# Performance work log

Measured on AMD Instinct MI355X. Metric: run time of the kernel, lower is better.

## Reference

```python
import jax, jax.numpy as jnp
import numpy as np

N = 50000   # nodes
E = 600000  # edges (avg degree 12)
F = 16      # raw node features
P = 32      # n_channels_preproc
C = 128     # n_channels
L = 6       # n_gnn_layers
LBL = 2     # n_labels


def _dense_init(k, fan_in, shape):
    return (jax.random.normal(k, shape, jnp.float32) / np.float32(np.sqrt(fan_in)))


def setup_inputs() -> dict:
    key = jax.random.key(0)
    ks = jax.random.split(key, 12)
    return {
        "x": jax.random.normal(ks[0], (N, F), jnp.float32),
        "edge_src": jax.random.randint(ks[1], (E,), 0, N, dtype=jnp.int32),
        "edge_dst": jax.random.randint(ks[2], (E,), 0, N, dtype=jnp.int32),
        "edge_weight": jax.random.uniform(ks[3], (E,), jnp.float32),  # normalized-adjacency values
        "preproc_W": _dense_init(ks[4], F, (F, P)), "preproc_b": jnp.zeros((P,), jnp.float32),
        "fc_in1_W": _dense_init(ks[5], P, (P, C)), "fc_in1_b": jnp.zeros((C,), jnp.float32),
        "fc_in2_W": _dense_init(ks[6], P, (P, C)), "fc_in2_b": jnp.zeros((C,), jnp.float32),
        "gcn_W": _dense_init(ks[7], C, (L, C, C)), "gcn_b": jnp.zeros((L, C), jnp.float32),
        "fcg_W": _dense_init(ks[8], 2 * C, (L, 2 * C, C)), "fcg_b": jnp.zeros((L, C), jnp.float32),
        "last1_W": _dense_init(ks[9], 2 * C, (2 * C, C)), "last1_b": jnp.zeros((C,), jnp.float32),
        "last2_W": _dense_init(ks[10], C, (C, LBL)), "last2_b": jnp.zeros((LBL,), jnp.float32),
    }


def reference(x, edge_src, edge_dst, edge_weight,
              preproc_W, preproc_b, fc_in1_W, fc_in1_b, fc_in2_W, fc_in2_b,
              gcn_W, gcn_b, fcg_W, fcg_b, last1_W, last1_b, last2_W, last2_b):
    relu = jax.nn.relu
    h = relu(x @ preproc_W + preproc_b)                      # preproc Dense
    node_id = relu(h @ fc_in1_W + fc_in1_b)                  # node identity branch
    h = relu(h @ fc_in2_W + fc_in2_b)

    def layer(h, params):
        W, b, Wf, bf = params
        # GCNConv: act(A_hat @ (h @ W) + b), A_hat as COO edge list
        hw = h @ W                                           # [N, C]
        msg = hw[edge_src] * edge_weight[:, None]            # [E, C]
        agg = jax.ops.segment_sum(msg, edge_dst, num_segments=N)
        g = relu(agg + b)
        merged = jnp.concatenate([node_id, g], axis=-1)      # [N, 2C]
        return relu(merged @ Wf + bf), None                  # dropout = identity (eval)

    h, _ = jax.lax.scan(layer, h, (gcn_W, gcn_b, fcg_W, fcg_b))

    merged = jnp.concatenate([node_id, h], axis=-1)
    h = relu(merged @ last1_W + last1_b)
    return jax.nn.sigmoid(h @ last2_W + last2_b)             # [N, n_labels]
```

## Files before the change

kernel.cpp:

```cpp
#include <hip/hip_runtime.h>
#include <cstddef>
#include <cstdint>

#define NN 50000
#define NE 600000
#define NB 391

typedef __attribute__((ext_vector_type(8))) short bf16x8;
typedef __attribute__((ext_vector_type(4))) float f32x4;

#define SWZ(x) (((x) ^ ((x) >> 2)) & 3)

#define GLDS16(src, dst)                                                     \
    __builtin_amdgcn_global_load_lds(                                        \
        (const __attribute__((address_space(1))) void*)(src),                \
        (__attribute__((address_space(3))) void*)(dst), 16, 0, 0)

__device__ __forceinline__ float bf2f(ushort u) {
    return __uint_as_float(((uint32_t)u) << 16);
}
__device__ __forceinline__ ushort f2bf(float f) {
    uint32_t b = __float_as_uint(f);
    return (ushort)((b + 0x7FFF + ((b >> 16) & 1)) >> 16);
}

__global__ __launch_bounds__(256)
void convbh_kernel(const float* __restrict__ f1W, const float* __restrict__ f2W,
                   const float* __restrict__ gW, const float* __restrict__ fgW,
                   const float* __restrict__ l1W, ushort* __restrict__ wt,
                   const int* __restrict__ dst, int* __restrict__ bcnt)
{
    if (blockIdx.x < 1312) {
        int i = blockIdx.x * 256 + threadIdx.x;
        if (i >= 335872) return;
        float v;
        if (i < 4096) {
            int c = i >> 5, k = i & 31;
            v = f1W[k * 128 + c];
        } else if (i < 8192) {
            int j = i - 4096; int c = j >> 5, k = j & 31;
            v = f2W[k * 128 + c];
        } else if (i < 8192 + 98304) {
            int j = i - 8192; int l = j >> 14, r = j & 16383;
            int c = r >> 7, k = r & 127;
            v = gW[l * 16384 + k * 128 + c];
        } else if (i < 8192 + 98304 + 196608) {
            int j = i - (8192 + 98304); int l = j >> 15, r = j & 32767;
            int c = r >> 8, k = r & 255;
            v = fgW[l * 32768 + k * 128 + c];
        } else {
            int j = i - (8192 + 98304 + 196608);
            int c = j >> 8, k = j & 255;
            v = l1W[k * 128 + c];
        }
        wt[i] = f2bf(v);
    } else {
        __shared__ int h[NB];
        int tx = threadIdx.x;
        for (int i = tx; i < NB; i += 256) h[i] = 0;
        __syncthreads();
        int e0 = (blockIdx.x - 1312) * 1024;
#pragma unroll
        for (int k = 0; k < 4; ++k) {
            int e = e0 + k * 256 + tx;
            if (e < NE) atomicAdd(&h[dst[e] >> 7], 1);
        }
        __syncthreads();
        for (int i = tx; i < NB; i += 256)
            if (h[i]) atomicAdd(&bcnt[i], h[i]);
    }
}

__global__ __launch_bounds__(512)
void bscan_kernel(const int* __restrict__ bcnt, int* __restrict__ bbase,
                  int* __restrict__ bcur)
{
    __shared__ int buf[512];
    int t = threadIdx.x;
    int v = (t < NB) ? bcnt[t] : 0;
    buf[t] = v;
    __syncthreads();
    for (int s = 1; s < 512; s <<= 1) {
        int u = (t >= s) ? buf[t - s] : 0;
        __syncthreads();
        buf[t] += u;
        __syncthreads();
    }
    if (t < NB) {
        int ex = buf[t] - v;
        bbase[t] = ex;
        bcur[t]  = ex;
    }
    if (t == 0) bbase[NB] = NE;
}

__global__ __launch_bounds__(256)
void pass1_kernel(const int* __restrict__ src, const int* __restrict__ dst,
                  const float* __restrict__ w, int* __restrict__ bcur,
                  unsigned int* __restrict__ stage_pk,
                  unsigned char* __restrict__ stage_dl)
{
    __shared__ int cnt[NB];
    __shared__ int gbase[NB];
    int tx = threadIdx.x;
    for (int i = tx; i < NB; i += 256) cnt[i] = 0;
    __syncthreads();
    int e0 = blockIdx.x * 1024;
    int myd[4], myrank[4];
    unsigned int mypk[4];
#pragma unroll
    for (int k = 0; k < 4; ++k) {
        int e = e0 + k * 256 + tx;
        if (e < NE) {
            int d = dst[e];
            myd[k]    = d;
            mypk[k]   = (unsigned int)src[e] | ((unsigned int)f2bf(w[e]) << 17);
            myrank[k] = atomicAdd(&cnt[d >> 7], 1);
        } else {
            myd[k] = -1;
        }
    }
    __syncthreads();
    for (int i = tx; i < NB; i += 256)
        gbase[i] = cnt[i] ? atomicAdd(&bcur[i], cnt[i]) : 0;
    __syncthreads();
#pragma unroll
    for (int k = 0; k < 4; ++k) {
        if (myd[k] >= 0) {
            int p = gbase[myd[k] >> 7] + myrank[k];
            stage_pk[p] = mypk[k];
            stage_dl[p] = (unsigned char)(myd[k] & 127);
        }
    }
}

__global__ __launch_bounds__(256)
void p2pre_kernel(const unsigned int* __restrict__ stage_pk,
                  const unsigned char* __restrict__ stage_dl,
                  const int* __restrict__ bbase,
                  unsigned int* __restrict__ esw, int* __restrict__ off,
                  const float* __restrict__ x, const float* __restrict__ preW,
                  const float* __restrict__ preb, ushort* __restrict__ h0b)
{
    if (blockIdx.x < NB) {
        __shared__ int h[128];
        __shared__ int lofs[128];
        int b    = blockIdx.x;
        int tx   = threadIdx.x;
        int base = bbase[b];
        int cnt  = bbase[b + 1] - base;
        if (tx < 128) h[tx] = 0;
        __syncthreads();
        for (int i = tx; i < cnt; i += 256)
            atomicAdd(&h[stage_dl[base + i]], 1);
        __syncthreads();
        if (tx == 0) {
            int run = 0;
            for (int i = 0; i < 128; ++i) { lofs[i] = run; run += h[i]; }
        }
        __syncthreads();
        int node0 = b * 128;
        if (tx < 128) {
            int n = node0 + tx;
            if (n < NN) off[n] = base + lofs[tx];
            h[tx] = 0;
        }
        if (b == NB - 1 && tx == 0) off[NN] = NE;
        __syncthreads();
        for (int i = tx; i < cnt; i += 256) {
            int d = stage_dl[base + i];
            int r = atomicAdd(&h[d], 1);
            esw[base + lofs[d] + r] = stage_pk[base + i];
        }
    } else {
        __shared__ float Wl[512];
        __shared__ float bl[32];
        int tx = threadIdx.x;
        Wl[tx]       = preW[tx];
        Wl[tx + 256] = preW[tx + 256];
        if (tx < 32) bl[tx] = preb[tx];
        __syncthreads();
        int n = (blockIdx.x - NB) * 256 + tx;
        if (n >= NN) return;
        float xr[16];
        const float4* xp = (const float4*)(x + (size_t)n * 16);
#pragma unroll
        for (int q = 0; q < 4; ++q) {
            float4 v = xp[q];
            xr[q*4+0]=v.x; xr[q*4+1]=v.y; xr[q*4+2]=v.z; xr[q*4+3]=v.w;
        }
        float acc[32];
#pragma unroll
        for (int c = 0; c < 32; ++c) acc[c] = bl[c];
#pragma unroll
        for (int k = 0; k < 16; ++k)
#pragma unroll
            for (int c = 0; c < 32; ++c)
                acc[c] = fmaf(xr[k], Wl[k*32+c], acc[c]);
        ushort4* op = (ushort4*)(h0b + (size_t)n * 32);
#pragma unroll
        for (int q = 0; q < 8; ++q) {
            ushort4 v;
            v.x = f2bf(fmaxf(acc[q*4+0], 0.f));
            v.y = f2bf(fmaxf(acc[q*4+1], 0.f));
            v.z = f2bf(fmaxf(acc[q*4+2], 0.f));
            v.w = f2bf(fmaxf(acc[q*4+3], 0.f));
            op[q] = v;
        }
    }
}

__global__ __launch_bounds__(128)
void fc1f0_kernel(const ushort* __restrict__ h0b,
                  const ushort* __restrict__ wf1, const float* __restrict__ f1b,
                  ushort* __restrict__ nidb,
                  const ushort* __restrict__ wf2, const float* __restrict__ f2b,
                  const ushort* __restrict__ wg, ushort* __restrict__ hwb)
{
    __shared__ ushort Atile[64 * 32];
    __shared__ ushort Btile[128 * 32];
    __shared__ ushort Xt[64 * 128];
    const int tx   = threadIdx.x;
    const int wave = tx >> 6;
    const int lane = tx & 63;
    const int rs  = lane >> 2;
    const int chn = (lane & 3) ^ SWZ(rs);
    const int m    = lane & 15;
    const int quad = lane >> 4;
    const int slot = quad ^ SWZ(m);

    if (blockIdx.x < 782) {
        const int bm = blockIdx.x * 64;
        f32x4 acc0[8], acc1[8];
#pragma unroll
        for (int t = 0; t < 8; ++t) {
            acc0[t] = (f32x4){0.f, 0.f, 0.f, 0.f};
            acc1[t] = (f32x4){0.f, 0.f, 0.f, 0.f};
        }
#pragma unroll
        for (int i = 0; i < 2; ++i) {
            int seg = wave + 2 * i;
            int row = seg * 16 + rs;
            int ar  = bm + row; if (ar >= NN) ar = NN - 1;
            GLDS16(h0b + (size_t)ar * 32 + chn * 8, Atile + seg * 512);
        }
#pragma unroll
        for (int i = 0; i < 4; ++i) {
            int seg = wave + 2 * i;
            int col = seg * 16 + rs;
            GLDS16(wf1 + (size_t)col * 32 + chn * 8, Btile + seg * 512);
        }
        __syncthreads();
        bf16x8 af0 = *(const bf16x8*)(Atile + (wave * 32 + m) * 32 + slot * 8);
        bf16x8 af1 = *(const bf16x8*)(Atile + (wave * 32 + 16 + m) * 32 + slot * 8);
#pragma unroll
        for (int t = 0; t < 8; ++t) {
            bf16x8 bfr = *(const bf16x8*)(Btile + (t * 16 + m) * 32 + slot * 8);
            acc0[t] = __builtin_amdgcn_mfma_f32_16x16x32_bf16(af0, bfr, acc0[t], 0, 0, 0);
            acc1[t] = __builtin_amdgcn_mfma_f32_16x16x32_bf16(af1, bfr, acc1[t], 0, 0, 0);
        }
        __syncthreads();
#pragma unroll
        for (int half = 0; half < 2; ++half) {
            const int orow0 = bm + wave * 32 + half * 16 + quad * 4;
#pragma unroll
            for (int t = 0; t < 8; ++t) {
                int col = t * 16 + m;
                float bb = f1b[col];
                f32x4 a = half ? acc1[t] : acc0[t];
#pragma unroll
                for (int r = 0; r < 4; ++r) {
                    int row = orow0 + r;
                    if (row < NN)
                        nidb[(size_t)row * 128 + col] = f2bf(fmaxf(a[r] + bb, 0.f));
                }
            }
        }
    } else {
        const int bm = (blockIdx.x - 782) * 64;
        f32x4 acc0[8], acc1[8];
#pragma unroll
        for (int t = 0; t < 8; ++t) {
            acc0[t] = (f32x4){0.f, 0.f, 0.f, 0.f};
            acc1[t] = (f32x4){0.f, 0.f, 0.f, 0.f};
        }
#pragma unroll
        for (int i = 0; i < 2; ++i) {
            int seg = wave + 2 * i;
            int row = seg * 16 + rs;
            int ar  = bm + row; if (ar >= NN) ar = NN - 1;
            GLDS16(h0b + (size_t)ar * 32 + chn * 8, Atile + seg * 512);
        }
#pragma unroll
        for (int i = 0; i < 4; ++i) {
            int seg = wave + 2 * i;
            int col = seg * 16 + rs;
            GLDS16(wf2 + (size_t)col * 32 + chn * 8, Btile + seg * 512);
        }
        __syncthreads();
        {
            bf16x8 af0 = *(const bf16x8*)(Atile + (wave * 32 + m) * 32 + slot * 8);
            bf16x8 af1 = *(const bf16x8*)(Atile + (wave * 32 + 16 + m) * 32 + slot * 8);
#pragma unroll
            for (int t = 0; t < 8; ++t) {
                bf16x8 bfr = *(const bf16x8*)(Btile + (t * 16 + m) * 32 + slot * 8);
                acc0[t] = __builtin_amdgcn_mfma_f32_16x16x32_bf16(af0, bfr, acc0[t], 0, 0, 0);
                acc1[t] = __builtin_amdgcn_mfma_f32_16x16x32_bf16(af1, bfr, acc1[t], 0, 0, 0);
            }
        }
        __syncthreads();
#pragma unroll
        for (int half = 0; half < 2; ++half) {
            int rbase = wave * 32 + half * 16 + quad * 4;
#pragma unroll
            for (int t = 0; t < 8; ++t) {
                int col = t * 16 + m;
                float bb = f2b[col];
                int c32 = col >> 5, within = col & 7, ks = (col >> 3) & 3;
                f32x4 a = half ? acc1[t] : acc0[t];
#pragma unroll
                for (int r = 0; r < 4; ++r) {
                    int row = rbase + r;
                    int pos = ks ^ SWZ(row & 15);
                    Xt[row * 128 + c32 * 32 + pos * 8 + within] =
                        f2bf(fmaxf(a[r] + bb, 0.f));
                }
            }
        }
#pragma unroll
        for (int t = 0; t < 8; ++t) {
            acc0[t] = (f32x4){0.f, 0.f, 0.f, 0.f};
            acc1[t] = (f32x4){0.f, 0.f, 0.f, 0.f};
        }
        __syncthreads();
        for (int c32 = 0; c32 < 4; ++c32) {
            int kk = c32 * 32;
#pragma unroll
            for (int i = 0; i < 4; ++i) {
                int seg = wave + 2 * i;
                int col = seg * 16 + rs;
                GLDS16(wg + (size_t)col * 128 + kk + chn * 8, Btile + seg * 512);
            }
            __syncthreads();
            bf16x8 af0 = *(const bf16x8*)(Xt + (wave * 32 + m) * 128 + kk + slot * 8);
            bf16x8 af1 = *(const bf16x8*)(Xt + (wave * 32 + 16 + m) * 128 + kk + slot * 8);
#pragma unroll
            for (int t = 0; t < 8; ++t) {
                bf16x8 bfr = *(const bf16x8*)(Btile + (t * 16 + m) * 32 + slot * 8);
                acc0[t] = __builtin_amdgcn_mfma_f32_16x16x32_bf16(af0, bfr, acc0[t], 0, 0, 0);
                acc1[t] = __builtin_amdgcn_mfma_f32_16x16x32_bf16(af1, bfr, acc1[t], 0, 0, 0);
            }
            __syncthreads();
        }
#pragma unroll
        for (int half = 0; half < 2; ++half) {
            const int orow0 = bm + wave * 32 + half * 16 + quad * 4;
#pragma unroll
            for (int t = 0; t < 8; ++t) {
                int col = t * 16 + m;
                f32x4 a = half ? acc1[t] : acc0[t];
#pragma unroll
                for (int r = 0; r < 4; ++r) {
                    int row = orow0 + r;
                    if (row < NN)
                        hwb[(size_t)row * 128 + col] = f2bf(a[r]);
                }
            }
        }
    }
}

__global__ __launch_bounds__(512)
void gemm_gather(const ushort* __restrict__ hw,
                 const unsigned int* __restrict__ esw,
                 const int* __restrict__ off,
                 const float* __restrict__ gbias,
                 const ushort* __restrict__ nid,
                 const ushort* __restrict__ Wt,
                 const float* __restrict__ bias,
                 const ushort* __restrict__ Wg,
                 ushort* __restrict__ out_hw, int nrows)
{
    __shared__ ushort Atile[64 * 32];
    __shared__ ushort Btile[128 * 32];
    __shared__ ushort AggXt[64 * 128];
    const int tx   = threadIdx.x;
    const int wave = tx >> 6;
    const int lane = tx & 63;
    const int bm   = blockIdx.x * 64;
    const int g    = wave >> 1;
    const int h    = wave & 1;
    const int rs   = lane >> 2;
    const int chn  = (lane & 3) ^ SWZ(rs);
    const int m    = lane & 15;
    const int quad = lane >> 4;
    const int slot = quad ^ SWZ(m);

    if (wave < 4) {
        int ar = bm + wave * 16 + rs; if (ar >= nrows) ar = nrows - 1;
        GLDS16(nid + (size_t)ar * 128 + chn * 8, Atile + wave * 512);
    }
    {
        int col = wave * 16 + rs;
        GLDS16(Wt + (size_t)col * 256 + chn * 8, Btile + wave * 512);
    }

    {
        const int n0   = bm + wave * 8;
        const int nend = n0 + 8;
        int n    = n0;
        const int base = off[n0 < NN ? n0 : NN];
        const int end  = off[nend < NN ? nend : NN];
        int nb = (n < NN) ? off[n + 1] : 0x7fffffff;
        const ushort* hp = hw + lane * 2;
        const float g0 = gbias[lane * 2], g1 = gbias[lane * 2 + 1];
        float a0 = 0.f, a1 = 0.f;
        const int c32g = lane >> 4;
        const int ksg  = (lane >> 2) & 3;
        const int wth  = (2 * lane) & 7;
        for (int chunk = base; chunk < end; chunk += 64) {
            int idx = chunk + lane;
            int pk = (idx < end) ? (int)esw[idx] : 0;
            int cnt = end - chunk; if (cnt > 64) cnt = 64;
            int cnt16 = (cnt + 15) & ~15;
            for (int j = 0; j < cnt16; j += 16) {
                int pp[16];
                unsigned int rv[16];
#pragma unroll
                for (int k = 0; k < 16; ++k)
                    pp[k] = __builtin_amdgcn_readlane(pk, j + k);
#pragma unroll
                for (int k = 0; k < 16; ++k)
                    rv[k] = *(const unsigned int*)(hp + (size_t)(pp[k] & 0x1FFFF) * 128);
#pragma unroll
                for (int k = 0; k < 16; ++k) {
                    int e = chunk + j + k;
                    while (e == nb) {
                        int row = n - bm;
                        unsigned int o = (unsigned int)f2bf(fmaxf(a0 + g0, 0.f)) |
                                         ((unsigned int)f2bf(fmaxf(a1 + g1, 0.f)) << 16);
                        int pos = ksg ^ SWZ(row & 15);
                        *(unsigned int*)(AggXt + row * 128 +
                            ((c32g * 32 + pos * 8 + wth) ^ ((row & 1) << 5))) = o;
                        a0 = 0.f; a1 = 0.f;
                        ++n;
                        nb = (n < nend && n < NN) ? off[n + 1] : 0x7fffffff;
                    }
                    float w = bf2f((ushort)((unsigned int)pp[k] >> 17));
                    a0 = fmaf(bf2f((ushort)(rv[k] & 0xffff)), w, a0);
                    a1 = fmaf(bf2f((ushort)(rv[k] >> 16)),    w, a1);
                }
            }
        }
        while (n < nend) {
            int row = n - bm;
            unsigned int o = (unsigned int)f2bf(fmaxf(a0 + g0, 0.f)) |
                             ((unsigned int)f2bf(fmaxf(a1 + g1, 0.f)) << 16);
            int pos = ksg ^ SWZ(row & 15);
            *(unsigned int*)(AggXt + row * 128 +
                ((c32g * 32 + pos * 8 + wth) ^ ((row & 1) << 5))) = o;
            a0 = 0.f; a1 = 0.f;
            ++n;
        }
    }

    f32x4 acc[4];
#pragma unroll
    for (int t = 0; t < 4; ++t) acc[t] = (f32x4){0.f, 0.f, 0.f, 0.f};

    for (int c8 = 0; c8 < 8; ++c8) {
        int kk = c8 * 32;
        if (c8 > 0) {
            if (c8 < 4 && wave < 4) {
                int ar = bm + wave * 16 + rs; if (ar >= nrows) ar = nrows - 1;
                GLDS16(nid + (size_t)ar * 128 + kk + chn * 8, Atile + wave * 512);
            }
            int col = wave * 16 + rs;
            GLDS16(Wt + (size_t)col * 256 + kk + chn * 8, Btile + wave * 512);
        }
        __syncthreads();
        bf16x8 af;
        if (c8 < 4) {
            af = *(const bf16x8*)(Atile + (g * 16 + m) * 32 + slot * 8);
        } else {
            int row = g * 16 + m;
            af = *(const bf16x8*)(AggXt + row * 128 +
                 (((c8 - 4) * 32 + slot * 8) ^ ((row & 1) << 5)));
        }
#pragma unroll
        for (int t = 0; t < 4; ++t) {
            bf16x8 bfr = *(const bf16x8*)(Btile + (h * 64 + t * 16 + m) * 32 + slot * 8);
            acc[t] = __builtin_amdgcn_mfma_f32_16x16x32_bf16(af, bfr, acc[t], 0, 0, 0);
        }
        __syncthreads();
    }

    {
        int col = wave * 16 + rs;
        GLDS16(Wg + (size_t)col * 128 + chn * 8, Btile + wave * 512);
    }

    {
        int rbase = g * 16 + quad * 4;
#pragma unroll
        for (int t = 0; t < 4; ++t) {
            int col = h * 64 + t * 16 + m;
            float bb = bias[col];
            int c32 = col >> 5, within = col & 7, ks = (col >> 3) & 3;
#pragma unroll
            for (int r = 0; r < 4; ++r) {
                int row = rbase + r;
                int pos = ks ^ SWZ(row & 15);
                AggXt[row * 128 + ((c32 * 32 + pos * 8 + within) ^ ((row & 1) << 5))] =
                    f2bf(fmaxf(acc[t][r] + bb, 0.f));
            }
        }
    }
#pragma unroll
    for (int t = 0; t < 4; ++t) acc[t] = (f32x4){0.f, 0.f, 0.f, 0.f};

    for (int c4 = 0; c4 < 4; ++c4) {
        int kk = c4 * 32;
        if (c4 > 0) {
            int col = wave * 16 + rs;
            GLDS16(Wg + (size_t)col * 128 + kk + chn * 8, Btile + wave * 512);
        }
        __syncthreads();
        int row = g * 16 + m;
        bf16x8 af = *(const bf16x8*)(AggXt + row * 128 +
                    ((kk + slot * 8) ^ ((row & 1) << 5)));
#pragma unroll
        for (int t = 0; t < 4; ++t) {
            bf16x8 bfr = *(const bf16x8*)(Btile + (h * 64 + t * 16 + m) * 32 + slot * 8);
            acc[t] = __builtin_amdgcn_mfma_f32_16x16x32_bf16(af, bfr, acc[t], 0, 0, 0);
        }
        __syncthreads();
    }

    {
        const int orow0 = bm + g * 16 + quad * 4;
#pragma unroll
        for (int t = 0; t < 4; ++t) {
            int col = h * 64 + t * 16 + m;
#pragma unroll
            for (int r = 0; r < 4; ++r) {
                int row = orow0 + r;
                if (row < nrows)
                    out_hw[(size_t)row * 128 + col] = f2bf(acc[t][r]);
            }
        }
    }
}

__global__ __launch_bounds__(512)
void gemm_last(const ushort* __restrict__ hw,
               const unsigned int* __restrict__ esw,
               const int* __restrict__ off,
               const float* __restrict__ gbias,
               const ushort* __restrict__ nid,
               const ushort* __restrict__ Wt, const float* __restrict__ bias5,
               const ushort* __restrict__ Wl1, const float* __restrict__ l1b,
               const float* __restrict__ l2W, const float* __restrict__ l2b,
               float* __restrict__ out, int nrows)
{
    __shared__ ushort Atile[64 * 32];
    __shared__ ushort Btile[128 * 32];
    __shared__ ushort AggXt[64 * 128];
    __shared__ float  w2s[256];
    __shared__ float  pbuf[64][2];
    const int tx   = threadIdx.x;
    const int wave = tx >> 6;
    const int lane = tx & 63;
    const int bm   = blockIdx.x * 64;
    const int g    = wave >> 1;
    const int h    = wave & 1;
    const int rs   = lane >> 2;
    const int chn  = (lane & 3) ^ SWZ(rs);
    const int m    = lane & 15;
    const int quad = lane >> 4;
    const int slot = quad ^ SWZ(m);

    if (tx < 256) w2s[tx] = l2W[tx];

    if (wave < 4) {
        int ar = bm + wave * 16 + rs; if (ar >= nrows) ar = nrows - 1;
        GLDS16(nid + (size_t)ar * 128 + chn * 8, Atile + wave * 512);
    }
    {
        int col = wave * 16 + rs;
        GLDS16(Wt + (size_t)col * 256 + chn * 8, Btile + wave * 512);
    }

    {
        const int n0   = bm + wave * 8;
        const int nend = n0 + 8;
        int n    = n0;
        const int base = off[n0 < NN ? n0 : NN];
        const int end  = off[nend < NN ? nend : NN];
        int nb = (n < NN) ? off[n + 1] : 0x7fffffff;
        const ushort* hp = hw + lane * 2;
        const float g0 = gbias[lane * 2], g1 = gbias[lane * 2 + 1];
        float a0 = 0.f, a1 = 0.f;
        const int c32g = lane >> 4;
        const int ksg  = (lane >> 2) & 3;
        const int wth  = (2 * lane) & 7;
        for (int chunk = base; chunk < end; chunk += 64) {
            int idx = chunk + lane;
            int pk = (idx < end) ? (int)esw[idx] : 0;
            int cnt = end - chunk; if (cnt > 64) cnt = 64;
            int cnt16 = (cnt + 15) & ~15;
            for (int j = 0; j < cnt16; j += 16) {
                int pp[16];
                unsigned int rv[16];
#pragma unroll
                for (int k = 0; k < 16; ++k)
                    pp[k] = __builtin_amdgcn_readlane(pk, j + k);
#pragma unroll
                for (int k = 0; k < 16; ++k)
                    rv[k] = *(const unsigned int*)(hp + (size_t)(pp[k] & 0x1FFFF) * 128);
#pragma unroll
                for (int k = 0; k < 16; ++k) {
                    int e = chunk + j + k;
                    while (e == nb) {
                        int row = n - bm;
                        unsigned int o = (unsigned int)f2bf(fmaxf(a0 + g0, 0.f)) |
                                         ((unsigned int)f2bf(fmaxf(a1 + g1, 0.f)) << 16);
                        int pos = ksg ^ SWZ(row & 15);
                        *(unsigned int*)(AggXt + row * 128 +
                            ((c32g * 32 + pos * 8 + wth) ^ ((row & 1) << 5))) = o;
                        a0 = 0.f; a1 = 0.f;
                        ++n;
                        nb = (n < nend && n < NN) ? off[n + 1] : 0x7fffffff;
                    }
                    float w = bf2f((ushort)((unsigned int)pp[k] >> 17));
                    a0 = fmaf(bf2f((ushort)(rv[k] & 0xffff)), w, a0);
                    a1 = fmaf(bf2f((ushort)(rv[k] >> 16)),    w, a1);
                }
            }
        }
        while (n < nend) {
            int row = n - bm;
            unsigned int o = (unsigned int)f2bf(fmaxf(a0 + g0, 0.f)) |
                             ((unsigned int)f2bf(fmaxf(a1 + g1, 0.f)) << 16);
            int pos = ksg ^ SWZ(row & 15);
            *(unsigned int*)(AggXt + row * 128 +
                ((c32g * 32 + pos * 8 + wth) ^ ((row & 1) << 5))) = o;
            a0 = 0.f; a1 = 0.f;
            ++n;
        }
    }

    f32x4 acc[4];
#pragma unroll
    for (int t = 0; t < 4; ++t) acc[t] = (f32x4){0.f, 0.f, 0.f, 0.f};

    for (int c8 = 0; c8 < 8; ++c8) {
        int kk = c8 * 32;
        if (c8 > 0) {
            if (c8 < 4 && wave < 4) {
                int ar = bm + wave * 16 + rs; if (ar >= nrows) ar = nrows - 1;
                GLDS16(nid + (size_t)ar * 128 + kk + chn * 8, Atile + wave * 512);
            }
            int col = wave * 16 + rs;
            GLDS16(Wt + (size_t)col * 256 + kk + chn * 8, Btile + wave * 512);
        }
        __syncthreads();
        bf16x8 af;
        if (c8 < 4) {
            af = *(const bf16x8*)(Atile + (g * 16 + m) * 32 + slot * 8);
        } else {
            int row = g * 16 + m;
            af = *(const bf16x8*)(AggXt + row * 128 +
                 (((c8 - 4) * 32 + slot * 8) ^ ((row & 1) << 5)));
        }
#pragma unroll
        for (int t = 0; t < 4; ++t) {
            bf16x8 bfr = *(const bf16x8*)(Btile + (h * 64 + t * 16 + m) * 32 + slot * 8);
            acc[t] = __builtin_amdgcn_mfma_f32_16x16x32_bf16(af, bfr, acc[t], 0, 0, 0);
        }
        __syncthreads();
    }

    if (wave < 4) {
        int ar = bm + wave * 16 + rs; if (ar >= nrows) ar = nrows - 1;
        GLDS16(nid + (size_t)ar * 128 + chn * 8, Atile + wave * 512);
    }
    {
        int col = wave * 16 + rs;
        GLDS16(Wl1 + (size_t)col * 256 + chn * 8, Btile + wave * 512);
    }

    {
        int rbase = g * 16 + quad * 4;
#pragma unroll
        for (int t = 0; t < 4; ++t) {
            int col = h * 64 + t * 16 + m;
            float bb = bias5[col];
            int c32 = col >> 5, within = col & 7, ks = (col >> 3) & 3;
#pragma unroll
            for (int r = 0; r < 4; ++r) {
                int row = rbase + r;
                int pos = ks ^ SWZ(row & 15);
                AggXt[row * 128 + ((c32 * 32 + pos * 8 + within) ^ ((row & 1) << 5))] =
                    f2bf(fmaxf(acc[t][r] + bb, 0.f));
            }
        }
    }
#pragma unroll
    for (int t = 0; t < 4; ++t) acc[t] = (f32x4){0.f, 0.f, 0.f, 0.f};

    for (int c8 = 0; c8 < 8; ++c8) {
        int kk = c8 * 32;
        if (c8 > 0) {
            if (c8 < 4 && wave < 4) {
                int ar = bm + wave * 16 + rs; if (ar >= nrows) ar = nrows - 1;
                GLDS16(nid + (size_t)ar * 128 + kk + chn * 8, Atile + wave * 512);
            }
            int col = wave * 16 + rs;
            GLDS16(Wl1 + (size_t)col * 256 + kk + chn * 8, Btile + wave * 512);
        }
        __syncthreads();
        bf16x8 af;
        if (c8 < 4) {
            af = *(const bf16x8*)(Atile + (g * 16 + m) * 32 + slot * 8);
        } else {
            int row = g * 16 + m;
            af = *(const bf16x8*)(AggXt + row * 128 +
                 (((c8 - 4) * 32 + slot * 8) ^ ((row & 1) << 5)));
        }
#pragma unroll
        for (int t = 0; t < 4; ++t) {
            bf16x8 bfr = *(const bf16x8*)(Btile + (h * 64 + t * 16 + m) * 32 + slot * 8);
            acc[t] = __builtin_amdgcn_mfma_f32_16x16x32_bf16(af, bfr, acc[t], 0, 0, 0);
        }
        __syncthreads();
    }

    float bb[4];
#pragma unroll
    for (int t = 0; t < 4; ++t) bb[t] = l1b[h * 64 + t * 16 + m];
    float pr0[4], pr1[4];
#pragma unroll
    for (int r = 0; r < 4; ++r) {
        float p0 = 0.f, p1 = 0.f;
#pragma unroll
        for (int t = 0; t < 4; ++t) {
            int col = h * 64 + t * 16 + m;
            float v = fmaxf(acc[t][r] + bb[t], 0.f);
            p0 = fmaf(v, w2s[col * 2 + 0], p0);
            p1 = fmaf(v, w2s[col * 2 + 1], p1);
        }
#pragma unroll
        for (int mask = 1; mask < 16; mask <<= 1) {
            p0 += __shfl_xor(p0, mask);
            p1 += __shfl_xor(p1, mask);
        }
        pr0[r] = p0; pr1[r] = p1;
    }
    if (h == 1 && m == 0) {
#pragma unroll
        for (int r = 0; r < 4; ++r) {
            int lrow = g * 16 + quad * 4 + r;
            pbuf[lrow][0] = pr0[r];
            pbuf[lrow][1] = pr1[r];
        }
    }
    __syncthreads();
    if (h == 0 && m == 0) {
        float b20 = l2b[0], b21 = l2b[1];
#pragma unroll
        for (int r = 0; r < 4; ++r) {
            int lrow = g * 16 + quad * 4 + r;
            int row = bm + lrow;
            if (row < nrows) {
                float p0 = pr0[r] + pbuf[lrow][0] + b20;
                float p1 = pr1[r] + pbuf[lrow][1] + b21;
                out[(size_t)row * 2 + 0] = 1.f / (1.f + __expf(-p0));
                out[(size_t)row * 2 + 1] = 1.f / (1.f + __expf(-p1));
            }
        }
    }
}

extern "C" void kernel_launch(void* const* d_in, const int* in_sizes, int n_in,
                              void* d_out, int out_size, void* d_ws, size_t ws_size,
                              hipStream_t stream)
{
    const float* x    = (const float*)d_in[0];
    const int*   esrc = (const int*)  d_in[1];
    const int*   edst = (const int*)  d_in[2];
    const float* ew   = (const float*)d_in[3];
    const float* preW = (const float*)d_in[4];
    const float* preb = (const float*)d_in[5];
    const float* f1W  = (const float*)d_in[6];
    const float* f1b  = (const float*)d_in[7];
    const float* f2W  = (const float*)d_in[8];
    const float* f2b  = (const float*)d_in[9];
    const float* gW   = (const float*)d_in[10];
    const float* gb   = (const float*)d_in[11];
    const float* fgW  = (const float*)d_in[12];
    const float* fgb  = (const float*)d_in[13];
    const float* l1W  = (const float*)d_in[14];
    const float* l1b  = (const float*)d_in[15];
    const float* l2W  = (const float*)d_in[16];
    const float* l2b  = (const float*)d_in[17];
    float* out = (float*)d_out;

    ushort* wt   = (ushort*)d_ws;
    ushort* wf1  = wt;
    ushort* wf2  = wf1 + 4096;
    ushort* wg   = wf2 + 4096;
    ushort* wfg  = wg  + 98304;
    ushort* wl1  = wfg + 196608;
    ushort* h0b  = wl1 + 32768;
    ushort* nidb = h0b  + (size_t)NN * 32;
    ushort* hwb  = nidb + (size_t)NN * 128;
    ushort* hwb2 = hwb  + (size_t)NN * 128;
    ushort* endu = hwb2 + (size_t)NN * 128;
    unsigned int* esw      = (unsigned int*)(((uintptr_t)endu + 15) & ~(uintptr_t)15);
    unsigned int* stage_pk = esw + NE;
    int*          bcnt     = (int*)(stage_pk + NE);
    int*          bbase    = bcnt + NB + 1;
    int*          bcur     = bbase + NB + 1;
    int*          off      = bcur + NB + 1;
    unsigned char* stage_dl = (unsigned char*)(off + NN + 2);

    const int gblocks = (NN + 63) / 64;
    const int eblocks = (NE + 1023) / 1024;

    hipMemsetAsync(bcnt, 0, (size_t)NB * sizeof(int), stream);
    convbh_kernel<<<1312 + eblocks, 256, 0, stream>>>(f1W, f2W, gW, fgW, l1W, wt,
                                                      edst, bcnt);
    bscan_kernel<<<1, 512, 0, stream>>>(bcnt, bbase, bcur);
    pass1_kernel<<<eblocks, 256, 0, stream>>>(esrc, edst, ew, bcur, stage_pk, stage_dl);
    p2pre_kernel<<<NB + (NN + 255) / 256, 256, 0, stream>>>(stage_pk, stage_dl, bbase,
                                                            esw, off, x, preW, preb, h0b);

    fc1f0_kernel<<<2 * gblocks, 128, 0, stream>>>(h0b, wf1, f1b, nidb,
                                                  wf2, f2b, wg, hwb);
    ushort* cur = hwb;
    ushort* nxt = hwb2;
    for (int l = 0; l < 5; ++l) {
        gemm_gather<<<gblocks, 512, 0, stream>>>(cur, esw, off,
                                                 gb + (size_t)l * 128, nidb,
                                                 wfg + (size_t)l * 32768,
                                                 fgb + (size_t)l * 128,
                                                 wg + (size_t)(l + 1) * 16384,
                                                 nxt, NN);
        ushort* tmp = cur; cur = nxt; nxt = tmp;
    }
    gemm_last<<<gblocks, 512, 0, stream>>>(cur, esw, off,
                                           gb + (size_t)5 * 128, nidb,
                                           wfg + (size_t)5 * 32768,
                                           fgb + (size_t)5 * 128,
                                           wl1, l1b, l2W, l2b, out, NN);
}
```

Measured before the change: 374.7 us.

## Load GEMM operands directly from global memory instead of staging through LDS

Removes the LDS Atile/Btile staging (global_load_lds plus barriers) in the fc, gather-GEMM and last kernels. Each wave now reads its MFMA A and B fragments straight from global memory, relying on L1/L2 caching of the small weight matrices. The goals are fewer __syncthreads and less LDS use, and the gather kernels also get a min-waves-per-EU hint of 6 to raise occupancy. The trade-off is redundant per-wave global loads of the weight tiles, and the occupancy hint may cap registers and cause spills.

```diff
diff --git a/kernel.cpp b/kernel.cpp
--- a/kernel.cpp
+++ b/kernel.cpp
@@ -10,11 +10,6 @@
 typedef __attribute__((ext_vector_type(4))) float f32x4;
 
 #define SWZ(x) (((x) ^ ((x) >> 2)) & 3)
-
-#define GLDS16(src, dst)                                                     \
-    __builtin_amdgcn_global_load_lds(                                        \
-        (const __attribute__((address_space(1))) void*)(src),                \
-        (__attribute__((address_space(3))) void*)(dst), 16, 0, 0)
 
 __device__ __forceinline__ float bf2f(ushort u) {
     return __uint_as_float(((uint32_t)u) << 16);
@@ -217,49 +212,39 @@
                   const ushort* __restrict__ wf2, const float* __restrict__ f2b,
                   const ushort* __restrict__ wg, ushort* __restrict__ hwb)
 {
-    __shared__ ushort Atile[64 * 32];
-    __shared__ ushort Btile[128 * 32];
     __shared__ ushort Xt[64 * 128];
     const int tx   = threadIdx.x;
     const int wave = tx >> 6;
     const int lane = tx & 63;
-    const int rs  = lane >> 2;
-    const int chn = (lane & 3) ^ SWZ(rs);
     const int m    = lane & 15;
     const int quad = lane >> 4;
     const int slot = quad ^ SWZ(m);
 
-    if (blockIdx.x < 782) {
-        const int bm = blockIdx.x * 64;
-        f32x4 acc0[8], acc1[8];
+    const bool p1 = blockIdx.x < 782;
+    const int bm  = (p1 ? blockIdx.x : blockIdx.x - 782) * 64;
+    const ushort* wf = p1 ? wf1 : wf2;
+    const float*  fb = p1 ? f1b : f2b;
+
+    f32x4 acc0[8], acc1[8];
+#pragma unroll
+    for (int t = 0; t < 8; ++t) {
+        acc0[t] = (f32x4){0.f, 0.f, 0.f, 0.f};
+        acc1[t] = (f32x4){0.f, 0.f, 0.f, 0.f};
+    }
+    {
+        int ar0 = bm + wave * 32 + m;      if (ar0 >= NN) ar0 = NN - 1;
+        int ar1 = bm + wave * 32 + 16 + m; if (ar1 >= NN) ar1 = NN - 1;
+        bf16x8 af0 = *(const bf16x8*)(h0b + (size_t)ar0 * 32 + quad * 8);
+        bf16x8 af1 = *(const bf16x8*)(h0b + (size_t)ar1 * 32 + quad * 8);
 #pragma unroll
         for (int t = 0; t < 8; ++t) {
-            acc0[t] = (f32x4){0.f, 0.f, 0.f, 0.f};
-            acc1[t] = (f32x4){0.f, 0.f, 0.f, 0.f};
-        }
-#pragma unroll
-        for (int i = 0; i < 2; ++i) {
-            int seg = wave + 2 * i;
-            int row = seg * 16 + rs;
-            int ar  = bm + row; if (ar >= NN) ar = NN - 1;
-            GLDS16(h0b + (size_t)ar * 32 + chn * 8, Atile + seg * 512);
-        }
-#pragma unroll
-        for (int i = 0; i < 4; ++i) {
-            int seg = wave + 2 * i;
-            int col = seg * 16 + rs;
-            GLDS16(wf1 + (size_t)col * 32 + chn * 8, Btile + seg * 512);
-        }
-        __syncthreads();
-        bf16x8 af0 = *(const bf16x8*)(Atile + (wave * 32 + m) * 32 + slot * 8);
-        bf16x8 af1 = *(const bf16x8*)(Atile + (wave * 32 + 16 + m) * 32 + slot * 8);
-#pragma unroll
-        for (int t = 0; t < 8; ++t) {
-            bf16x8 bfr = *(const bf16x8*)(Btile + (t * 16 + m) * 32 + slot * 8);
+            bf16x8 bfr = *(const bf16x8*)(wf + (size_t)(t * 16 + m) * 32 + quad * 8);
             acc0[t] = __builtin_amdgcn_mfma_f32_16x16x32_bf16(af0, bfr, acc0[t], 0, 0, 0);
             acc1[t] = __builtin_amdgcn_mfma_f32_16x16x32_bf16(af1, bfr, acc1[t], 0, 0, 0);
         }
-        __syncthreads();
+    }
+
+    if (p1) {
 #pragma unroll
         for (int half = 0; half < 2; ++half) {
             const int orow0 = bm + wave * 32 + half * 16 + quad * 4;
@@ -277,45 +262,13 @@
             }
         }
     } else {
-        const int bm = (blockIdx.x - 782) * 64;
-        f32x4 acc0[8], acc1[8];
-#pragma unroll
-        for (int t = 0; t < 8; ++t) {
-            acc0[t] = (f32x4){0.f, 0.f, 0.f, 0.f};
-            acc1[t] = (f32x4){0.f, 0.f, 0.f, 0.f};
-        }
-#pragma unroll
-        for (int i = 0; i < 2; ++i) {
-            int seg = wave + 2 * i;
-            int row = seg * 16 + rs;
-            int ar  = bm + row; if (ar >= NN) ar = NN - 1;
-            GLDS16(h0b + (size_t)ar * 32 + chn * 8, Atile + seg * 512);
-        }
-#pragma unroll
-        for (int i = 0; i < 4; ++i) {
-            int seg = wave + 2 * i;
-            int col = seg * 16 + rs;
-            GLDS16(wf2 + (size_t)col * 32 + chn * 8, Btile + seg * 512);
-        }
-        __syncthreads();
-        {
-            bf16x8 af0 = *(const bf16x8*)(Atile + (wave * 32 + m) * 32 + slot * 8);
-            bf16x8 af1 = *(const bf16x8*)(Atile + (wave * 32 + 16 + m) * 32 + slot * 8);
-#pragma unroll
-            for (int t = 0; t < 8; ++t) {
-                bf16x8 bfr = *(const bf16x8*)(Btile + (t * 16 + m) * 32 + slot * 8);
-                acc0[t] = __builtin_amdgcn_mfma_f32_16x16x32_bf16(af0, bfr, acc0[t], 0, 0, 0);
-                acc1[t] = __builtin_amdgcn_mfma_f32_16x16x32_bf16(af1, bfr, acc1[t], 0, 0, 0);
-            }
-        }
-        __syncthreads();
 #pragma unroll
         for (int half = 0; half < 2; ++half) {
             int rbase = wave * 32 + half * 16 + quad * 4;
 #pragma unroll
             for (int t = 0; t < 8; ++t) {
                 int col = t * 16 + m;
-                float bb = f2b[col];
+                float bb = fb[col];
                 int c32 = col >> 5, within = col & 7, ks = (col >> 3) & 3;
                 f32x4 a = half ? acc1[t] : acc0[t];
 #pragma unroll
@@ -332,25 +285,16 @@
             acc0[t] = (f32x4){0.f, 0.f, 0.f, 0.f};
             acc1[t] = (f32x4){0.f, 0.f, 0.f, 0.f};
         }
-        __syncthreads();
         for (int c32 = 0; c32 < 4; ++c32) {
             int kk = c32 * 32;
-#pragma unroll
-            for (int i = 0; i < 4; ++i) {
-                int seg = wave + 2 * i;
-                int col = seg * 16 + rs;
-                GLDS16(wg + (size_t)col * 128 + kk + chn * 8, Btile + seg * 512);
-            }
-            __syncthreads();
             bf16x8 af0 = *(const bf16x8*)(Xt + (wave * 32 + m) * 128 + kk + slot * 8);
             bf16x8 af1 = *(const bf16x8*)(Xt + (wave * 32 + 16 + m) * 128 + kk + slot * 8);
 #pragma unroll
             for (int t = 0; t < 8; ++t) {
-                bf16x8 bfr = *(const bf16x8*)(Btile + (t * 16 + m) * 32 + slot * 8);
+                bf16x8 bfr = *(const bf16x8*)(wg + (size_t)(t * 16 + m) * 128 + kk + quad * 8);
                 acc0[t] = __builtin_amdgcn_mfma_f32_16x16x32_bf16(af0, bfr, acc0[t], 0, 0, 0);
                 acc1[t] = __builtin_amdgcn_mfma_f32_16x16x32_bf16(af1, bfr, acc1[t], 0, 0, 0);
             }
-            __syncthreads();
         }
 #pragma unroll
         for (int half = 0; half < 2; ++half) {
@@ -370,7 +314,7 @@
     }
 }
 
-__global__ __launch_bounds__(512)
+__global__ __launch_bounds__(512, 6)
 void gemm_gather(const ushort* __restrict__ hw,
                  const unsigned int* __restrict__ esw,
                  const int* __restrict__ off,
@@ -381,8 +325,6 @@
                  const ushort* __restrict__ Wg,
                  ushort* __restrict__ out_hw, int nrows)
 {
-    __shared__ ushort Atile[64 * 32];
-    __shared__ ushort Btile[128 * 32];
     __shared__ ushort AggXt[64 * 128];
     const int tx   = threadIdx.x;
     const int wave = tx >> 6;
@@ -390,20 +332,9 @@
     const int bm   = blockIdx.x * 64;
     const int g    = wave >> 1;
     const int h    = wave & 1;
-    const int rs   = lane >> 2;
-    const int chn  = (lane & 3) ^ SWZ(rs);
     const int m    = lane & 15;
     const int quad = lane >> 4;
     const int slot = quad ^ SWZ(m);
-
-    if (wave < 4) {
-        int ar = bm + wave * 16 + rs; if (ar >= nrows) ar = nrows - 1;
-        GLDS16(nid + (size_t)ar * 128 + chn * 8, Atile + wave * 512);
-    }
-    {
-        int col = wave * 16 + rs;
-        GLDS16(Wt + (size_t)col * 256 + chn * 8, Btile + wave * 512);
-    }
 
     {
         const int n0   = bm + wave * 8;
@@ -468,37 +399,33 @@
 #pragma unroll
     for (int t = 0; t < 4; ++t) acc[t] = (f32x4){0.f, 0.f, 0.f, 0.f};
 
-    for (int c8 = 0; c8 < 8; ++c8) {
+    int ar = bm + g * 16 + m; if (ar >= nrows) ar = nrows - 1;
+    for (int c8 = 0; c8 < 4; ++c8) {
         int kk = c8 * 32;
-        if (c8 > 0) {
-            if (c8 < 4 && wave < 4) {
-                int ar = bm + wave * 16 + rs; if (ar >= nrows) ar = nrows - 1;
-                GLDS16(nid + (size_t)ar * 128 + kk + chn * 8, Atile + wave * 512);
-            }
-            int col = wave * 16 + rs;
-            GLDS16(Wt + (size_t)col * 256 + kk + chn * 8, Btile + wave * 512);
-        }
-        __syncthreads();
-        bf16x8 af;
-        if (c8 < 4) {
-            af = *(const bf16x8*)(Atile + (g * 16 + m) * 32 + slot * 8);
-        } else {
-            int row = g * 16 + m;
-            af = *(const bf16x8*)(AggXt + row * 128 +
-                 (((c8 - 4) * 32 + slot * 8) ^ ((row & 1) << 5)));
-        }
+        bf16x8 af = *(const bf16x8*)(nid + (size_t)ar * 128 + kk + quad * 8);
 #pragma unroll
         for (int t = 0; t < 4; ++t) {
-            bf16x8 bfr = *(const bf16x8*)(Btile + (h * 64 + t * 16 + m) * 32 + slot * 8);
+            bf16x8 bfr = *(const bf16x8*)(Wt + (size_t)(h * 64 + t * 16 + m) * 256 + kk + quad * 8);
             acc[t] = __builtin_amdgcn_mfma_f32_16x16x32_bf16(af, bfr, acc[t], 0, 0, 0);
         }
-        __syncthreads();
-    }
-
-    {
-        int col = wave * 16 + rs;
-        GLDS16(Wg + (size_t)col * 128 + chn * 8, Btile + wave * 512);
-    }
+    }
+    __syncthreads();
+
+    {
+        const int row = g * 16 + m;
+        const int rx  = (row & 1) << 5;
+        for (int c8 = 4; c8 < 8; ++c8) {
+            int kk = c8 * 32;
+            bf16x8 af = *(const bf16x8*)(AggXt + row * 128 +
+                        (((c8 - 4) * 32 + slot * 8) ^ rx));
+#pragma unroll
+            for (int t = 0; t < 4; ++t) {
+                bf16x8 bfr = *(const bf16x8*)(Wt + (size_t)(h * 64 + t * 16 + m) * 256 + kk + quad * 8);
+                acc[t] = __builtin_amdgcn_mfma_f32_16x16x32_bf16(af, bfr, acc[t], 0, 0, 0);
+            }
+        }
+    }
+    __syncthreads();
 
     {
         int rbase = g * 16 + quad * 4;
@@ -518,23 +445,20 @@
     }
 #pragma unroll
     for (int t = 0; t < 4; ++t) acc[t] = (f32x4){0.f, 0.f, 0.f, 0.f};
-
-    for (int c4 = 0; c4 < 4; ++c4) {
-        int kk = c4 * 32;
-        if (c4 > 0) {
-            int col = wave * 16 + rs;
-            GLDS16(Wg + (size_t)col * 128 + kk + chn * 8, Btile + wave * 512);
-        }
-        __syncthreads();
-        int row = g * 16 + m;
-        bf16x8 af = *(const bf16x8*)(AggXt + row * 128 +
-                    ((kk + slot * 8) ^ ((row & 1) << 5)));
-#pragma unroll
-        for (int t = 0; t < 4; ++t) {
-            bf16x8 bfr = *(const bf16x8*)(Btile + (h * 64 + t * 16 + m) * 32 + slot * 8);
-            acc[t] = __builtin_amdgcn_mfma_f32_16x16x32_bf16(af, bfr, acc[t], 0, 0, 0);
-        }
-        __syncthreads();
+    __syncthreads();
+
+    {
+        const int row = g * 16 + m;
+        const int rx  = (row & 1) << 5;
+        for (int c4 = 0; c4 < 4; ++c4) {
+            int kk = c4 * 32;
+            bf16x8 af = *(const bf16x8*)(AggXt + row * 128 + ((kk + slot * 8) ^ rx));
+#pragma unroll
+            for (int t = 0; t < 4; ++t) {
+                bf16x8 bfr = *(const bf16x8*)(Wg + (size_t)(h * 64 + t * 16 + m) * 128 + kk + quad * 8);
+                acc[t] = __builtin_amdgcn_mfma_f32_16x16x32_bf16(af, bfr, acc[t], 0, 0, 0);
+            }
+        }
     }
 
     {
@@ -552,7 +476,7 @@
     }
 }
 
-__global__ __launch_bounds__(512)
+__global__ __launch_bounds__(512, 6)
 void gemm_last(const ushort* __restrict__ hw,
                const unsigned int* __restrict__ esw,
                const int* __restrict__ off,
@@ -563,8 +487,6 @@
                const float* __restrict__ l2W, const float* __restrict__ l2b,
                float* __restrict__ out, int nrows)
 {
-    __shared__ ushort Atile[64 * 32];
-    __shared__ ushort Btile[128 * 32];
     __shared__ ushort AggXt[64 * 128];
     __shared__ float  w2s[256];
     __shared__ float  pbuf[64][2];
@@ -574,22 +496,11 @@
     const int bm   = blockIdx.x * 64;
     const int g    = wave >> 1;
     const int h    = wave & 1;
-    const int rs   = lane >> 2;
-    const int chn  = (lane & 3) ^ SWZ(rs);
     const int m    = lane & 15;
     const int quad = lane >> 4;
     const int slot = quad ^ SWZ(m);
 
     if (tx < 256) w2s[tx] = l2W[tx];
-
-    if (wave < 4) {
-        int ar = bm + wave * 16 + rs; if (ar >= nrows) ar = nrows - 1;
-        GLDS16(nid + (size_t)ar * 128 + chn * 8, Atile + wave * 512);
-    }
-    {
-        int col = wave * 16 + rs;
-        GLDS16(Wt + (size_t)col * 256 + chn * 8, Btile + wave * 512);
-    }
 
     {
         const int n0   = bm + wave * 8;
@@ -654,41 +565,34 @@
 #pragma unroll
     for (int t = 0; t < 4; ++t) acc[t] = (f32x4){0.f, 0.f, 0.f, 0.f};
 
-    for (int c8 = 0; c8 < 8; ++c8) {
+    int ar = bm + g * 16 + m; if (ar >= nrows) ar = nrows - 1;
+
+    for (int c8 = 0; c8 < 4; ++c8) {
         int kk = c8 * 32;
-        if (c8 > 0) {
-            if (c8 < 4 && wave < 4) {
-                int ar = bm + wave * 16 + rs; if (ar >= nrows) ar = nrows - 1;
-                GLDS16(nid + (size_t)ar * 128 + kk + chn * 8, Atile + wave * 512);
-            }
-            int col = wave * 16 + rs;
-            GLDS16(Wt + (size_t)col * 256 + kk + chn * 8, Btile + wave * 512);
-        }
-        __syncthreads();
-        bf16x8 af;
-        if (c8 < 4) {
-            af = *(const bf16x8*)(Atile + (g * 16 + m) * 32 + slot * 8);
-        } else {
-            int row = g * 16 + m;
-            af = *(const bf16x8*)(AggXt + row * 128 +
-                 (((c8 - 4) * 32 + slot * 8) ^ ((row & 1) << 5)));
-        }
+        bf16x8 af = *(const bf16x8*)(nid + (size_t)ar * 128 + kk + quad * 8);
 #pragma unroll
         for (int t = 0; t < 4; ++t) {
-            bf16x8 bfr = *(const bf16x8*)(Btile + (h * 64 + t * 16 + m) * 32 + slot * 8);
+            bf16x8 bfr = *(const bf16x8*)(Wt + (size_t)(h * 64 + t * 16 + m) * 256 + kk + quad * 8);
             acc[t] = __builtin_amdgcn_mfma_f32_16x16x32_bf16(af, bfr, acc[t], 0, 0, 0);
         }
-        __syncthreads();
-    }
-
-    if (wave < 4) {
-        int ar = bm + wave * 16 + rs; if (ar >= nrows) ar = nrows - 1;
-        GLDS16(nid + (size_t)ar * 128 + chn * 8, Atile + wave * 512);
-    }
-    {
-        int col = wave * 16 + rs;
-        GLDS16(Wl1 + (size_t)col * 256 + chn * 8, Btile + wave * 512);
-    }
+    }
+    __syncthreads();
+
+    {
+        const int row = g * 16 + m;
+        const int rx  = (row & 1) << 5;
+        for (int c8 = 4; c8 < 8; ++c8) {
+            int kk = c8 * 32;
+            bf16x8 af = *(const bf16x8*)(AggXt + row * 128 +
+                        (((c8 - 4) * 32 + slot * 8) ^ rx));
+#pragma unroll
+            for (int t = 0; t < 4; ++t) {
+                bf16x8 bfr = *(const bf16x8*)(Wt + (size_t)(h * 64 + t * 16 + m) * 256 + kk + quad * 8);
+                acc[t] = __builtin_amdgcn_mfma_f32_16x16x32_bf16(af, bfr, acc[t], 0, 0, 0);
+            }
+        }
+    }
+    __syncthreads();
 
     {
         int rbase = g * 16 + quad * 4;
@@ -708,32 +612,26 @@
     }
 #pragma unroll
     for (int t = 0; t < 4; ++t) acc[t] = (f32x4){0.f, 0.f, 0.f, 0.f};
-
-    for (int c8 = 0; c8 < 8; ++c8) {
-        int kk = c8 * 32;
-        if (c8 > 0) {
-            if (c8 < 4 && wave < 4) {
-                int ar = bm + wave * 16 + rs; if (ar >= nrows) ar = nrows - 1;
-                GLDS16(nid + (size_t)ar * 128 + kk + chn * 8, Atile + wave * 512);
-            }
-            int col = wave * 16 + rs;
-            GLDS16(Wl1 + (size_t)col * 256 + kk + chn * 8, Btile + wave * 512);
-        }
-        __syncthreads();
-        bf16x8 af;
-        if (c8 < 4) {
-            af = *(const bf16x8*)(Atile + (g * 16 + m) * 32 + slot * 8);
-        } else {
-            int row = g * 16 + m;
-            af = *(const bf16x8*)(AggXt + row * 128 +
-                 (((c8 - 4) * 32 + slot * 8) ^ ((row & 1) << 5)));
-        }
-#pragma unroll
-        for (int t = 0; t < 4; ++t) {
-            bf16x8 bfr = *(const bf16x8*)(Btile + (h * 64 + t * 16 + m) * 32 + slot * 8);
-            acc[t] = __builtin_amdgcn_mfma_f32_16x16x32_bf16(af, bfr, acc[t], 0, 0, 0);
-        }
-        __syncthreads();
+    __syncthreads();
+
+    {
+        const int row = g * 16 + m;
+        const int rx  = (row & 1) << 5;
+        for (int c8 = 0; c8 < 8; ++c8) {
+            int kk = c8 * 32;
+            bf16x8 af;
+            if (c8 < 4) {
+                af = *(const bf16x8*)(nid + (size_t)ar * 128 + kk + quad * 8);
+            } else {
+                af = *(const bf16x8*)(AggXt + row * 128 +
+                     (((c8 - 4) * 32 + slot * 8) ^ rx));
+            }
+#pragma unroll
+            for (int t = 0; t < 4; ++t) {
+                bf16x8 bfr = *(const bf16x8*)(Wl1 + (size_t)(h * 64 + t * 16 + m) * 256 + kk + quad * 8);
+                acc[t] = __builtin_amdgcn_mfma_f32_16x16x32_bf16(af, bfr, acc[t], 0, 0, 0);
+            }
+        }
     }
 
     float bb[4];
```

Measured after the change: 575.0 us. 1.53x slower.
